# Kernel tuning notes

Measured on AMD Instinct MI355X. Metric: run time of the kernel, lower is better.

Reference implementation:

```python
import jax, jax.numpy as jnp
import numpy as np

EPS = 1e-5

def _ln(x, g, b):
    mu = jnp.mean(x, axis=-1, keepdims=True)
    var = jnp.mean((x - mu) ** 2, axis=-1, keepdims=True)
    return (x - mu) * jax.lax.rsqrt(var + EPS) * g + b

def _leaky(x):
    return jax.nn.leaky_relu(x, 0.1)

def _gather(feats, idx):
    # feats: [B,N,C], idx: [B,M,K] -> [B,M,K,C]
    return jax.vmap(lambda f, i: f[i])(feats, idx)

def _forward(dense_xyz, dense_feats, pe_w1, pe_b1, pe_g1, pe_be1, pe_w2, pe_b2, pe_g2, pe_be2,
             wn_w1, wn_b1, wn_g1, wn_be1, wn_w2, wn_b2, wn_g2, wn_be2, wn_w3, wn_b3, wn_g3, wn_be3,
             nm_g, nm_b, l1_w, l1_b, l2_w, l2_b, sc_w, sc_b, nei_inds):
    gathered_xyz = _gather(dense_xyz, nei_inds)             # [B,M,K,3]
    localized = gathered_xyz - dense_xyz[:, :, None, :]     # relative coords (no subsampling: M==N)
    # pe_convs WeightNet: 3 -> 32 -> 32, LayerNorm per layer, LeakyReLU(0.1) except last
    h = _leaky(_ln(localized @ pe_w1 + pe_b1, pe_g1, pe_be1))
    feat_pe = _ln(h @ pe_w2 + pe_b2, pe_g2, pe_be2)         # [B,M,K,32]
    # weightnet: 3 -> 16 -> 16 -> Cin (per-edge depthwise weights)
    w = _leaky(_ln(localized @ wn_w1 + wn_b1, wn_g1, wn_be1))
    w = _leaky(_ln(w @ wn_w2 + wn_b2, wn_g2, wn_be2))
    w = _ln(w @ wn_w3 + wn_b3, wn_g3, wn_be3)               # [B,M,K,Cin]
    gathered_feat = _gather(dense_feats, nei_inds)          # [B,M,K,Cin]
    # depthwise aggregation over K, pe channels aggregated alongside
    agg = jnp.concatenate([jnp.sum(gathered_feat * w, axis=2), jnp.sum(feat_pe, axis=2)], axis=-1)
    x = _ln(agg, nm_g, nm_b)                                # LayerNorm(Cin+32)
    x = _leaky(x @ l1_w + l1_b)                             # inverted bottleneck 288 -> 1024
    x = x @ l2_w + l2_b                                     # 1024 -> Cout
    shortcut = dense_feats @ sc_w + sc_b                    # unary shortcut Cin -> Cout
    return _leaky(shortcut + x)

def setup_inputs():
    key = jax.random.key(0)
    B, N, K, CIN, COUT, PE, H = 1, 32768, 16, 256, 512, 32, 16
    ks = jax.random.split(key, 12)
    def g(k, shape, s=0.02):
        return jax.random.normal(k, shape, dtype=jnp.float32) * s
    return {
        "dense_xyz": jax.random.uniform(ks[0], (B, N, 3), dtype=jnp.float32),
        "dense_feats": jax.random.normal(ks[1], (B, N, CIN), dtype=jnp.float32),
        "nei_inds": jax.random.randint(ks[2], (B, N, K), 0, N),
        "pe_w1": g(ks[3], (3, PE), 0.2), "pe_b1": jnp.zeros((PE,), jnp.float32),
        "pe_g1": jnp.ones((PE,), jnp.float32), "pe_be1": jnp.zeros((PE,), jnp.float32),
        "pe_w2": g(ks[4], (PE, PE), 0.1), "pe_b2": jnp.zeros((PE,), jnp.float32),
        "pe_g2": jnp.ones((PE,), jnp.float32), "pe_be2": jnp.zeros((PE,), jnp.float32),
        "wn_w1": g(ks[5], (3, H), 0.2), "wn_b1": jnp.zeros((H,), jnp.float32),
        "wn_g1": jnp.ones((H,), jnp.float32), "wn_be1": jnp.zeros((H,), jnp.float32),
        "wn_w2": g(ks[6], (H, H), 0.1), "wn_b2": jnp.zeros((H,), jnp.float32),
        "wn_g2": jnp.ones((H,), jnp.float32), "wn_be2": jnp.zeros((H,), jnp.float32),
        "wn_w3": g(ks[7], (H, CIN), 0.1), "wn_b3": jnp.zeros((CIN,), jnp.float32),
        "wn_g3": jnp.ones((CIN,), jnp.float32), "wn_be3": jnp.zeros((CIN,), jnp.float32),
        "nm_g": jnp.ones((CIN + PE,), jnp.float32), "nm_b": jnp.zeros((CIN + PE,), jnp.float32),
        "l1_w": g(ks[8], (CIN + PE, 4 * CIN)), "l1_b": jnp.zeros((4 * CIN,), jnp.float32),
        "l2_w": g(ks[9], (4 * CIN, COUT)), "l2_b": jnp.zeros((COUT,), jnp.float32),
        "sc_w": g(ks[10], (CIN, COUT)), "sc_b": jnp.zeros((COUT,), jnp.float32),
    }

def reference(dense_xyz, dense_feats, nei_inds, pe_w1, pe_b1, pe_g1, pe_be1, pe_w2, pe_b2, pe_g2, pe_be2,
              wn_w1, wn_b1, wn_g1, wn_be1, wn_w2, wn_b2, wn_g2, wn_be2, wn_w3, wn_b3, wn_g3, wn_be3,
              nm_g, nm_b, l1_w, l1_b, l2_w, l2_b, sc_w, sc_b):
    return _forward(dense_xyz, dense_feats, pe_w1, pe_b1, pe_g1, pe_be1, pe_w2, pe_b2, pe_g2, pe_be2,
                    wn_w1, wn_b1, wn_g1, wn_be1, wn_w2, wn_b2, wn_g2, wn_be2, wn_w3, wn_b3, wn_g3, wn_be3,
                    nm_g, nm_b, l1_w, l1_b, l2_w, l2_b, sc_w, sc_b, nei_inds)
```

## Files before the change

kernel.cpp:

```cpp
#include <hip/hip_runtime.h>

#define NPTS  32768
#define KNB   16
#define CINC  256
#define PEC   32
#define HWN   16
#define CMID  288
#define L1OUT 1024
#define COUTC 512
#define EPSLN 1e-5f
#define PBLK  16
#define W2LD  272

typedef __attribute__((ext_vector_type(8))) short short8;
typedef __attribute__((ext_vector_type(4))) float f32x4;
typedef __attribute__((ext_vector_type(2))) float f32x2;

__device__ __forceinline__ float leaky(float x) { return x > 0.f ? x : 0.1f * x; }

__device__ __forceinline__ float bf2f(unsigned short u) {
    union { unsigned int i; float f; } x; x.i = ((unsigned int)u) << 16; return x.f;
}
__device__ __forceinline__ unsigned short f2bf(float f) {
    unsigned int x = __float_as_uint(f);
    x = (x + 0x7fffu + ((x >> 16) & 1u)) >> 16;
    return (unsigned short)x;
}

__device__ __forceinline__ f32x2 lo2(f32x4 v) { return __builtin_shufflevector(v, v, 0, 1); }
__device__ __forceinline__ f32x2 hi2(f32x4 v) { return __builtin_shufflevector(v, v, 2, 3); }

__device__ __forceinline__ void pkfma(f32x2& d, f32x2 a, f32x2 b) {
    asm("v_pk_fma_f32 %0, %1, %2, %0" : "+v"(d) : "v"(a), "v"(b));
}
__device__ __forceinline__ void pkfma_lo(f32x2& d, f32x2 a, f32x2 b) {
    asm("v_pk_fma_f32 %0, %1, %2, %0 op_sel:[0,0,0] op_sel_hi:[0,1,1]" : "+v"(d) : "v"(a), "v"(b));
}
__device__ __forceinline__ void pkfma_hi(f32x2& d, f32x2 a, f32x2 b) {
    asm("v_pk_fma_f32 %0, %1, %2, %0 op_sel:[1,0,0] op_sel_hi:[1,1,1]" : "+v"(d) : "v"(a), "v"(b));
}
__device__ __forceinline__ void pkfma_lo_s(f32x2& d, f32x2 a, f32x2 b) {
    asm("v_pk_fma_f32 %0, %1, %2, %0 op_sel:[0,0,0] op_sel_hi:[0,1,1]" : "+v"(d) : "v"(a), "s"(b));
}
__device__ __forceinline__ void pkfma_hi_s(f32x2& d, f32x2 a, f32x2 b) {
    asm("v_pk_fma_f32 %0, %1, %2, %0 op_sel:[1,0,0] op_sel_hi:[1,1,1]" : "+v"(d) : "v"(a), "s"(b));
}
__device__ __forceinline__ void pkfma_s0(f32x2& d, f32x2 a, f32x2 b) {
    asm("v_pk_fma_f32 %0, %1, %2, %0" : "+v"(d) : "s"(a), "v"(b));
}

__device__ __forceinline__ void gld_lds16(const unsigned short* g, unsigned short* l) {
    __builtin_amdgcn_global_load_lds(
        (const __attribute__((address_space(1))) unsigned int*)g,
        (__attribute__((address_space(3))) unsigned int*)l,
        16, 0, 0);
}
__device__ __forceinline__ void gld_lds16f(const float* g, float* l) {
    __builtin_amdgcn_global_load_lds(
        (const __attribute__((address_space(1))) unsigned int*)g,
        (__attribute__((address_space(3))) unsigned int*)l,
        16, 0, 0);
}

__device__ __forceinline__ void stage_tile(const unsigned short* __restrict__ g,
                                           size_t ld, int row0, int k0,
                                           unsigned short* lds, int wave, int lane)
{
    #pragma unroll
    for (int r = 0; r < 2; ++r) {
        int e   = r * 2048 + wave * 512 + lane * 8;
        int row = e >> 5;
        int kp  = e & 31;
        int kl  = kp ^ ((row & 3) << 3);
        const unsigned short* src = g + (size_t)(row0 + row) * ld + (k0 + kl);
        gld_lds16(src, lds + r * 2048 + wave * 512);
    }
}

__global__ __launch_bounds__(256) void wn3_stats_kernel(
    const float* __restrict__ W3, const float* __restrict__ b3, float* __restrict__ st)
{
    const int b = blockIdx.x;
    const int t = threadIdx.x;
    const int lane = t & 63, wave = t >> 6;
    const int c0 = lane * 4;

    if (b < 64) {
        int pair = b * 4 + wave;
        int h = pair >> 4, hp = pair & 15;
        f32x4 a  = *(const f32x4*)(W3 + h * CINC + c0);
        f32x4 bb = *(const f32x4*)(W3 + hp * CINC + c0);
        float g = a[0] * bb[0] + a[1] * bb[1] + a[2] * bb[2] + a[3] * bb[3];
        #pragma unroll
        for (int off = 1; off < 64; off <<= 1) g += __shfl_xor(g, off);
        if (lane == 0) st[pair] = g * (1.f / CINC);
    } else if (b == 64) {
        #pragma unroll
        for (int i = 0; i < 4; ++i) {
            int h = wave * 4 + i;
            f32x4 w  = *(const f32x4*)(W3 + h * CINC + c0);
            f32x4 bb = *(const f32x4*)(b3 + c0);
            float s  = w[0] + w[1] + w[2] + w[3];
            float sb = w[0] * bb[0] + w[1] * bb[1] + w[2] * bb[2] + w[3] * bb[3];
            #pragma unroll
            for (int off = 1; off < 64; off <<= 1) { s += __shfl_xor(s, off); sb += __shfl_xor(sb, off); }
            if (lane == 0) { st[256 + h] = s * (1.f / CINC); st[272 + h] = sb * (1.f / CINC); }
        }
    } else if (wave == 0) {
        f32x4 bb = *(const f32x4*)(b3 + c0);
        float s = bb[0] + bb[1] + bb[2] + bb[3];
        float q = bb[0] * bb[0] + bb[1] * bb[1] + bb[2] * bb[2] + bb[3] * bb[3];
        #pragma unroll
        for (int off = 1; off < 64; off <<= 1) { s += __shfl_xor(s, off); q += __shfl_xor(q, off); }
        if (lane == 0) { st[288] = s * (1.f / CINC); st[289] = q * (1.f / CINC); }
    }
}

__global__ __launch_bounds__(256, 3) void edge_fused_kernel(
    const float* __restrict__ xyz, const unsigned short* __restrict__ featsb,
    const int* __restrict__ nei,
    const float* __restrict__ pe_w1, const float* __restrict__ pe_b1,
    const float* __restrict__ pe_g1, const float* __restrict__ pe_be1,
    const float* __restrict__ pe_w2, const float* __restrict__ pe_b2,
    const float* __restrict__ pe_g2, const float* __restrict__ pe_be2,
    const float* __restrict__ wn_w1, const float* __restrict__ wn_b1,
    const float* __restrict__ wn_g1, const float* __restrict__ wn_be1,
    const float* __restrict__ wn_w2, const float* __restrict__ wn_b2,
    const float* __restrict__ wn_g2, const float* __restrict__ wn_be2,
    const float* __restrict__ st,
    const float* __restrict__ wn_w3, const float* __restrict__ wn_b3,
    const float* __restrict__ wn_g3, const float* __restrict__ wn_be3,
    const float* __restrict__ nm_g, const float* __restrict__ nm_b,
    unsigned short* __restrict__ xln)
{
    __shared__ __align__(16) float W3s[16 * 256];
    __shared__ __align__(16) float w2s[PBLK * W2LD];
    __shared__ __align__(16) float rms[PBLK * 16];
    __shared__ __align__(16) float mus[PBLK * 16];
    __shared__ float pes[PBLK * 32];

    const int t = threadIdx.x;

    {
        const int lane = t & 63, wave = t >> 6;
        #pragma unroll
        for (int r = 0; r < 4; ++r) {
            int base = (wave * 4 + r) * 256;
            gld_lds16f(wn_w3 + base + lane * 4, W3s + base);
        }
    }

    {
        const int lp = t >> 4, kk = t & 15;
        const int m = blockIdx.x * PBLK + lp;
        const int n = nei[m * KNB + kk];
        const float lx = xyz[n * 3 + 0] - xyz[m * 3 + 0];
        const float ly = xyz[n * 3 + 1] - xyz[m * 3 + 1];
        const float lz = xyz[n * 3 + 2] - xyz[m * 3 + 2];

        f32x2 w1p[8];
        float s = 0.f, q = 0.f;
        #pragma unroll
        for (int c4 = 0; c4 < 4; ++c4) {
            f32x4 wa = *(const f32x4*)&wn_w1[c4 * 4];
            f32x4 wb = *(const f32x4*)&wn_w1[16 + c4 * 4];
            f32x4 wc = *(const f32x4*)&wn_w1[32 + c4 * 4];
            f32x4 bb = *(const f32x4*)&wn_b1[c4 * 4];
            #pragma unroll
            for (int j = 0; j < 4; ++j) {
                float v = bb[j] + lx * wa[j] + ly * wb[j] + lz * wc[j];
                int c = c4 * 4 + j;
                w1p[c >> 1][c & 1] = v; s += v; q += v * v;
            }
        }
        float mu = s * (1.f / 16.f);
        float rstd = rsqrtf(q * (1.f / 16.f) - mu * mu + EPSLN);
        #pragma unroll
        for (int c4 = 0; c4 < 4; ++c4) {
            f32x4 g = *(const f32x4*)&wn_g1[c4 * 4];
            f32x4 be = *(const f32x4*)&wn_be1[c4 * 4];
            #pragma unroll
            for (int j = 0; j < 4; ++j) {
                int c = c4 * 4 + j;
                w1p[c >> 1][c & 1] = leaky((w1p[c >> 1][c & 1] - mu) * rstd * g[j] + be[j]);
            }
        }

        f32x2 w2p[8];
        #pragma unroll
        for (int c4 = 0; c4 < 4; ++c4) {
            f32x4 bb = *(const f32x4*)&wn_b2[c4 * 4];
            w2p[c4 * 2] = lo2(bb); w2p[c4 * 2 + 1] = hi2(bb);
        }
        #pragma unroll 2
        for (int jp = 0; jp < 8; ++jp) {
            f32x2 hp = w1p[jp];
            #pragma unroll
            for (int c4 = 0; c4 < 4; ++c4) {
                f32x4 w = *(const f32x4*)&wn_w2[(2 * jp) * 16 + c4 * 4];
                pkfma_lo_s(w2p[c4 * 2], hp, lo2(w));
                pkfma_lo_s(w2p[c4 * 2 + 1], hp, hi2(w));
            }
            #pragma unroll
            for (int c4 = 0; c4 < 4; ++c4) {
                f32x4 w = *(const f32x4*)&wn_w2[(2 * jp + 1) * 16 + c4 * 4];
                pkfma_hi_s(w2p[c4 * 2], hp, lo2(w));
                pkfma_hi_s(w2p[c4 * 2 + 1], hp, hi2(w));
            }
        }
        s = 0.f; q = 0.f;
        #pragma unroll
        for (int i = 0; i < 8; ++i) {
            s += w2p[i][0] + w2p[i][1];
            q += w2p[i][0] * w2p[i][0] + w2p[i][1] * w2p[i][1];
        }
        mu = s * (1.f / 16.f);
        rstd = rsqrtf(q * (1.f / 16.f) - mu * mu + EPSLN);
        #pragma unroll
        for (int c4 = 0; c4 < 4; ++c4) {
            f32x4 g = *(const f32x4*)&wn_g2[c4 * 4];
            f32x4 be = *(const f32x4*)&wn_be2[c4 * 4];
            #pragma unroll
            for (int j = 0; j < 4; ++j) {
                int c = c4 * 4 + j;
                w2p[c >> 1][c & 1] = leaky((w2p[c >> 1][c & 1] - mu) * rstd * g[j] + be[j]);
            }
        }

        float mu3 = st[288];
        #pragma unroll
        for (int h4 = 0; h4 < 4; ++h4) {
            f32x4 wm = *(const f32x4*)&st[256 + h4 * 4];
            mu3 += wm[0] * w2p[h4 * 2][0] + wm[1] * w2p[h4 * 2][1]
                 + wm[2] * w2p[h4 * 2 + 1][0] + wm[3] * w2p[h4 * 2 + 1][1];
        }
        float esq = st[289];
        #pragma unroll 4
        for (int hh = 0; hh < 16; ++hh) {
            f32x2 acc2 = {0.f, 0.f};
            #pragma unroll
            for (int h4 = 0; h4 < 4; ++h4) {
                f32x4 g = *(const f32x4*)&st[hh * 16 + h4 * 4];
                pkfma_s0(acc2, lo2(g), w2p[h4 * 2]);
                pkfma_s0(acc2, hi2(g), w2p[h4 * 2 + 1]);
            }
            float acc = acc2[0] + acc2[1] + 2.f * st[272 + hh];
            esq += w2p[hh >> 1][hh & 1] * acc;
        }
        float r3 = rsqrtf(esq - mu3 * mu3 + EPSLN);

        #pragma unroll
        for (int hh = 0; hh < 16; ++hh)
            w2s[lp * W2LD + hh * 16 + kk] = w2p[hh >> 1][hh & 1];
        rms[lp * 16 + kk] = r3;
        mus[lp * 16 + kk] = mu3;

        f32x2 h2[16];
        s = 0.f; q = 0.f;
        #pragma unroll
        for (int c4 = 0; c4 < 8; ++c4) {
            f32x4 wa = *(const f32x4*)&pe_w1[c4 * 4];
            f32x4 wb = *(const f32x4*)&pe_w1[32 + c4 * 4];
            f32x4 wc = *(const f32x4*)&pe_w1[64 + c4 * 4];
            f32x4 bb = *(const f32x4*)&pe_b1[c4 * 4];
            #pragma unroll
            for (int j = 0; j < 4; ++j) {
                float v = bb[j] + lx * wa[j] + ly * wb[j] + lz * wc[j];
                int c = c4 * 4 + j;
                h2[c >> 1][c & 1] = v; s += v; q += v * v;
            }
        }
        mu = s * (1.f / 32.f);
        rstd = rsqrtf(q * (1.f / 32.f) - mu * mu + EPSLN);
        #pragma unroll
        for (int c4 = 0; c4 < 8; ++c4) {
            f32x4 g = *(const f32x4*)&pe_g1[c4 * 4];
            f32x4 be = *(const f32x4*)&pe_be1[c4 * 4];
            #pragma unroll
            for (int j = 0; j < 4; ++j) {
                int c = c4 * 4 + j;
                h2[c >> 1][c & 1] = leaky((h2[c >> 1][c & 1] - mu) * rstd * g[j] + be[j]);
            }
        }

        f32x2 f2[16];
        #pragma unroll
        for (int c4 = 0; c4 < 8; ++c4) {
            f32x4 bb = *(const f32x4*)&pe_b2[c4 * 4];
            f2[c4 * 2] = lo2(bb); f2[c4 * 2 + 1] = hi2(bb);
        }
        #pragma unroll 2
        for (int jp = 0; jp < 16; ++jp) {
            f32x2 hp = h2[jp];
            #pragma unroll
            for (int c4 = 0; c4 < 8; ++c4) {
                f32x4 w = *(const f32x4*)&pe_w2[(2 * jp) * 32 + c4 * 4];
                pkfma_lo_s(f2[c4 * 2], hp, lo2(w));
                pkfma_lo_s(f2[c4 * 2 + 1], hp, hi2(w));
            }
            #pragma unroll
            for (int c4 = 0; c4 < 8; ++c4) {
                f32x4 w = *(const f32x4*)&pe_w2[(2 * jp + 1) * 32 + c4 * 4];
                pkfma_hi_s(f2[c4 * 2], hp, lo2(w));
                pkfma_hi_s(f2[c4 * 2 + 1], hp, hi2(w));
            }
        }
        s = 0.f; q = 0.f;
        #pragma unroll
        for (int i = 0; i < 16; ++i) {
            s += f2[i][0] + f2[i][1];
            q += f2[i][0] * f2[i][0] + f2[i][1] * f2[i][1];
        }
        mu = s * (1.f / 32.f);
        rstd = rsqrtf(q * (1.f / 32.f) - mu * mu + EPSLN);
        #pragma unroll
        for (int c4 = 0; c4 < 8; ++c4) {
            f32x4 g = *(const f32x4*)&pe_g2[c4 * 4];
            f32x4 be = *(const f32x4*)&pe_be2[c4 * 4];
            #pragma unroll
            for (int j = 0; j < 4; ++j) {
                int c = c4 * 4 + j;
                float v = (f2[c >> 1][c & 1] - mu) * rstd * g[j] + be[j];
                v += __shfl_xor(v, 1);
                v += __shfl_xor(v, 2);
                v += __shfl_xor(v, 4);
                v += __shfl_xor(v, 8);
                if (kk == 0) pes[lp * 32 + c] = v;
            }
        }
    }
    __syncthreads();

    const int lane = t & 63, wave = t >> 6;
    const int c0 = lane * 4;
    const f32x4 b3r  = *(const f32x4*)(wn_b3 + c0);
    const f32x4 g3r  = *(const f32x4*)(wn_g3 + c0);
    const f32x4 be3r = *(const f32x4*)(wn_be3 + c0);

    for (int pp = 0; pp < 4; ++pp) {
        const int lp = wave * 4 + pp;
        const int p  = blockIdx.x * PBLK + lp;
        const int* np = nei + p * KNB;

        f32x2 raw2[16][2];
        #pragma unroll
        for (int k = 0; k < 16; ++k) {
            raw2[k][0] = (f32x2){0.f, 0.f};
            raw2[k][1] = (f32x2){0.f, 0.f};
        }

        #pragma unroll 2
        for (int hh = 0; hh < 16; ++hh) {
            f32x4 w3r = *(const f32x4*)&W3s[hh * 256 + c0];
            f32x2 w01 = lo2(w3r), w23 = hi2(w3r);
            f32x4 u0 = *(const f32x4*)&w2s[lp * W2LD + hh * 16 + 0];
            f32x4 u1 = *(const f32x4*)&w2s[lp * W2LD + hh * 16 + 4];
            f32x4 u2 = *(const f32x4*)&w2s[lp * W2LD + hh * 16 + 8];
            f32x4 u3 = *(const f32x4*)&w2s[lp * W2LD + hh * 16 + 12];
            f32x2 p0 = lo2(u0), p1 = hi2(u0), p2 = lo2(u1), p3 = hi2(u1);
            f32x2 p4 = lo2(u2), p5 = hi2(u2), p6 = lo2(u3), p7 = hi2(u3);
            pkfma_lo(raw2[ 0][0], p0, w01); pkfma_lo(raw2[ 0][1], p0, w23);
            pkfma_hi(raw2[ 1][0], p0, w01); pkfma_hi(raw2[ 1][1], p0, w23);
            pkfma_lo(raw2[ 2][0], p1, w01); pkfma_lo(raw2[ 2][1], p1, w23);
            pkfma_hi(raw2[ 3][0], p1, w01); pkfma_hi(raw2[ 3][1], p1, w23);
            pkfma_lo(raw2[ 4][0], p2, w01); pkfma_lo(raw2[ 4][1], p2, w23);
            pkfma_hi(raw2[ 5][0], p2, w01); pkfma_hi(raw2[ 5][1], p2, w23);
            pkfma_lo(raw2[ 6][0], p3, w01); pkfma_lo(raw2[ 6][1], p3, w23);
            pkfma_hi(raw2[ 7][0], p3, w01); pkfma_hi(raw2[ 7][1], p3, w23);
            pkfma_lo(raw2[ 8][0], p4, w01); pkfma_lo(raw2[ 8][1], p4, w23);
            pkfma_hi(raw2[ 9][0], p4, w01); pkfma_hi(raw2[ 9][1], p4, w23);
            pkfma_lo(raw2[10][0], p5, w01); pkfma_lo(raw2[10][1], p5, w23);
            pkfma_hi(raw2[11][0], p5, w01); pkfma_hi(raw2[11][1], p5, w23);
            pkfma_lo(raw2[12][0], p6, w01); pkfma_lo(raw2[12][1], p6, w23);
            pkfma_hi(raw2[13][0], p6, w01); pkfma_hi(raw2[13][1], p6, w23);
            pkfma_lo(raw2[14][0], p7, w01); pkfma_lo(raw2[14][1], p7, w23);
            pkfma_hi(raw2[15][0], p7, w01); pkfma_hi(raw2[15][1], p7, w23);
        }

        float agg[4] = {0.f, 0.f, 0.f, 0.f};
        #pragma unroll
        for (int k4 = 0; k4 < 4; ++k4) {
            f32x4 rkv = *(const f32x4*)&rms[lp * 16 + k4 * 4];
            f32x4 muv = *(const f32x4*)&mus[lp * 16 + k4 * 4];
            #pragma unroll
            for (int r = 0; r < 4; ++r) {
                int k = k4 * 4 + r;
                int nk = np[k];
                float rk  = rkv[r];
                float muk = muv[r];
                ushort4 fu = *(const ushort4*)(featsb + (size_t)nk * CINC + c0);
                float w3x = (raw2[k][0][0] + b3r[0] - muk) * rk * g3r[0] + be3r[0];
                float w3y = (raw2[k][0][1] + b3r[1] - muk) * rk * g3r[1] + be3r[1];
                float w3z = (raw2[k][1][0] + b3r[2] - muk) * rk * g3r[2] + be3r[2];
                float w3w = (raw2[k][1][1] + b3r[3] - muk) * rk * g3r[3] + be3r[3];
                agg[0] += bf2f(fu.x) * w3x;
                agg[1] += bf2f(fu.y) * w3y;
                agg[2] += bf2f(fu.z) * w3z;
                agg[3] += bf2f(fu.w) * w3w;
            }
        }

        float pv = (lane < 32) ? pes[lp * 32 + lane] : 0.f;

        float s = agg[0] + agg[1] + agg[2] + agg[3];
        float q = agg[0] * agg[0] + agg[1] * agg[1] + agg[2] * agg[2] + agg[3] * agg[3];
        if (lane < 32) { s += pv; q += pv * pv; }
        #pragma unroll
        for (int off = 1; off < 64; off <<= 1) {
            s += __shfl_xor(s, off);
            q += __shfl_xor(q, off);
        }
        float mu = s * (1.f / 288.f);
        float rstd = rsqrtf(q * (1.f / 288.f) - mu * mu + EPSLN);

        f32x4 ngr = *(const f32x4*)(nm_g + c0);
        f32x4 nbr = *(const f32x4*)(nm_b + c0);
        unsigned short* xp = xln + (size_t)p * CMID;
        ushort4 o;
        o.x = f2bf((agg[0] - mu) * rstd * ngr[0] + nbr[0]);
        o.y = f2bf((agg[1] - mu) * rstd * ngr[1] + nbr[1]);
        o.z = f2bf((agg[2] - mu) * rstd * ngr[2] + nbr[2]);
        o.w = f2bf((agg[3] - mu) * rstd * ngr[3] + nbr[3]);
        *(ushort4*)(xp + c0) = o;
        if (lane < 32)
            xp[256 + lane] = f2bf((pv - mu) * rstd * nm_g[256 + lane] + nm_b[256 + lane]);
    }
}

__global__ __launch_bounds__(256) void transpose_bf16_kernel(
    const float* __restrict__ src, unsigned short* __restrict__ dst, int K, int N)
{
    __shared__ float tile[32][33];
    const int k0 = blockIdx.y * 32, n0 = blockIdx.x * 32;
    const int tx = threadIdx.x & 31, ty = threadIdx.x >> 5;
    #pragma unroll
    for (int i = ty; i < 32; i += 8)
        tile[i][tx] = src[(size_t)(k0 + i) * N + n0 + tx];
    __syncthreads();
    #pragma unroll
    for (int i = ty; i < 32; i += 8)
        dst[(size_t)(n0 + i) * K + k0 + tx] = f2bf(tile[tx][i]);
}

__global__ __launch_bounds__(256) void feats_bf16_kernel(
    const float* __restrict__ src, unsigned short* __restrict__ dst)
{
    int i = (blockIdx.x * 256 + threadIdx.x) * 4;
    float4 v = *(const float4*)(src + i);
    ushort4 o;
    o.x = f2bf(v.x); o.y = f2bf(v.y); o.z = f2bf(v.z); o.w = f2bf(v.w);
    *(ushort4*)(dst + i) = o;
}

__global__ __launch_bounds__(256) void gemm1_mfma(
    const unsigned short* __restrict__ A,
    const unsigned short* __restrict__ BT,
    const float* __restrict__ bias,
    unsigned short* __restrict__ C)
{
    __shared__ unsigned short As[128 * 32];
    __shared__ unsigned short Bs[128 * 32];
    const int t = threadIdx.x;
    const int lane = t & 63, wave = t >> 6;
    const int wm = wave >> 1, wn = wave & 1;
    const int m0 = blockIdx.y * 128, n0 = blockIdx.x * 128;
    const int l15 = lane & 15, j0 = (lane >> 4) << 3;

    f32x4 zero = {0.f, 0.f, 0.f, 0.f};
    f32x4 acc[4][4];
    #pragma unroll
    for (int i = 0; i < 4; ++i)
        #pragma unroll
        for (int j = 0; j < 4; ++j) acc[i][j] = zero;

    for (int kt = 0; kt < CMID; kt += 32) {
        stage_tile(A,  CMID, m0, kt, As, wave, lane);
        stage_tile(BT, CMID, n0, kt, Bs, wave, lane);
        __syncthreads();
        short8 af[4], bf[4];
        #pragma unroll
        for (int i = 0; i < 4; ++i) {
            int ar = wm * 64 + i * 16 + l15;
            af[i] = *(const short8*)&As[ar * 32 + (j0 ^ ((ar & 3) << 3))];
            int br = wn * 64 + i * 16 + l15;
            bf[i] = *(const short8*)&Bs[br * 32 + (j0 ^ ((br & 3) << 3))];
        }
        #pragma unroll
        for (int i = 0; i < 4; ++i)
            #pragma unroll
            for (int j = 0; j < 4; ++j)
                acc[i][j] = __builtin_amdgcn_mfma_f32_16x16x32_bf16(af[i], bf[j], acc[i][j], 0, 0, 0);
        __syncthreads();
    }

    const int q = lane >> 4;
    #pragma unroll
    for (int j = 0; j < 4; ++j) {
        int ncol = n0 + wn * 64 + j * 16 + l15;
        float bv = bias[ncol];
        #pragma unroll
        for (int i = 0; i < 4; ++i) {
            int mbase = m0 + wm * 64 + i * 16 + q * 4;
            #pragma unroll
            for (int r = 0; r < 4; ++r)
                C[(size_t)(mbase + r) * L1OUT + ncol] = f2bf(leaky(acc[i][j][r] + bv));
        }
    }
}

__global__ __launch_bounds__(256) void gemm2_mfma(
    const unsigned short* __restrict__ H,
    const unsigned short* __restrict__ W2T,
    const unsigned short* __restrict__ F,
    const unsigned short* __restrict__ WscT,
    const float* __restrict__ b2, const float* __restrict__ bsc,
    float* __restrict__ Out)
{
    __shared__ unsigned short As[128 * 32];
    __shared__ unsigned short Bs[128 * 32];
    const int t = threadIdx.x;
    const int lane = t & 63, wave = t >> 6;
    const int wm = wave >> 1, wn = wave & 1;
    const int m0 = blockIdx.y * 128, n0 = blockIdx.x * 128;
    const int l15 = lane & 15, j0 = (lane >> 4) << 3;

    f32x4 zero = {0.f, 0.f, 0.f, 0.f};
    f32x4 acc[4][4];
    #pragma unroll
    for (int i = 0; i < 4; ++i)
        #pragma unroll
        for (int j = 0; j < 4; ++j) acc[i][j] = zero;

    for (int kt = 0; kt < L1OUT; kt += 32) {
        stage_tile(H,   L1OUT, m0, kt, As, wave, lane);
        stage_tile(W2T, L1OUT, n0, kt, Bs, wave, lane);
        __syncthreads();
        short8 af[4], bf[4];
        #pragma unroll
        for (int i = 0; i < 4; ++i) {
            int ar = wm * 64 + i * 16 + l15;
            af[i] = *(const short8*)&As[ar * 32 + (j0 ^ ((ar & 3) << 3))];
            int br = wn * 64 + i * 16 + l15;
            bf[i] = *(const short8*)&Bs[br * 32 + (j0 ^ ((br & 3) << 3))];
        }
        #pragma unroll
        for (int i = 0; i < 4; ++i)
            #pragma unroll
            for (int j = 0; j < 4; ++j)
                acc[i][j] = __builtin_amdgcn_mfma_f32_16x16x32_bf16(af[i], bf[j], acc[i][j], 0, 0, 0);
        __syncthreads();
    }
    for (int kt = 0; kt < CINC; kt += 32) {
        stage_tile(F,    CINC, m0, kt, As, wave, lane);
        stage_tile(WscT, CINC, n0, kt, Bs, wave, lane);
        __syncthreads();
        short8 af[4], bf[4];
        #pragma unroll
        for (int i = 0; i < 4; ++i) {
            int ar = wm * 64 + i * 16 + l15;
            af[i] = *(const short8*)&As[ar * 32 + (j0 ^ ((ar & 3) << 3))];
            int br = wn * 64 + i * 16 + l15;
            bf[i] = *(const short8*)&Bs[br * 32 + (j0 ^ ((br & 3) << 3))];
        }
        #pragma unroll
        for (int i = 0; i < 4; ++i)
            #pragma unroll
            for (int j = 0; j < 4; ++j)
                acc[i][j] = __builtin_amdgcn_mfma_f32_16x16x32_bf16(af[i], bf[j], acc[i][j], 0, 0, 0);
        __syncthreads();
    }

    const int q = lane >> 4;
    #pragma unroll
    for (int j = 0; j < 4; ++j) {
        int ncol = n0 + wn * 64 + j * 16 + l15;
        float bv = b2[ncol] + bsc[ncol];
        #pragma unroll
        for (int i = 0; i < 4; ++i) {
            int mbase = m0 + wm * 64 + i * 16 + q * 4;
            #pragma unroll
            for (int r = 0; r < 4; ++r)
                Out[(size_t)(mbase + r) * COUTC + ncol] = leaky(acc[i][j][r] + bv);
        }
    }
}

extern "C" void kernel_launch(void* const* d_in, const int* in_sizes, int n_in,
                              void* d_out, int out_size, void* d_ws, size_t ws_size,
                              hipStream_t stream)
{
    const float* xyz    = (const float*)d_in[0];
    const float* feats  = (const float*)d_in[1];
    const int*   nei    = (const int*)d_in[2];
    const float* pe_w1  = (const float*)d_in[3];
    const float* pe_b1  = (const float*)d_in[4];
    const float* pe_g1  = (const float*)d_in[5];
    const float* pe_be1 = (const float*)d_in[6];
    const float* pe_w2  = (const float*)d_in[7];
    const float* pe_b2  = (const float*)d_in[8];
    const float* pe_g2  = (const float*)d_in[9];
    const float* pe_be2 = (const float*)d_in[10];
    const float* wn_w1  = (const float*)d_in[11];
    const float* wn_b1  = (const float*)d_in[12];
    const float* wn_g1  = (const float*)d_in[13];
    const float* wn_be1 = (const float*)d_in[14];
    const float* wn_w2  = (const float*)d_in[15];
    const float* wn_b2  = (const float*)d_in[16];
    const float* wn_g2  = (const float*)d_in[17];
    const float* wn_be2 = (const float*)d_in[18];
    const float* wn_w3  = (const float*)d_in[19];
    const float* wn_b3  = (const float*)d_in[20];
    const float* wn_g3  = (const float*)d_in[21];
    const float* wn_be3 = (const float*)d_in[22];
    const float* nm_g   = (const float*)d_in[23];
    const float* nm_b   = (const float*)d_in[24];
    const float* l1_w   = (const float*)d_in[25];
    const float* l1_b   = (const float*)d_in[26];
    const float* l2_w   = (const float*)d_in[27];
    const float* l2_b   = (const float*)d_in[28];
    const float* sc_w   = (const float*)d_in[29];
    const float* sc_b   = (const float*)d_in[30];

    char* ws = (char*)d_ws;
    unsigned short* xln    = (unsigned short*)(ws);
    unsigned short* featsb = (unsigned short*)(ws + 18874368);
    unsigned short* l1_wT  = (unsigned short*)(ws + 35651584);
    unsigned short* l2_wT  = (unsigned short*)(ws + 36241408);
    unsigned short* sc_wT  = (unsigned short*)(ws + 37289984);
    float*          st     = (float*)(ws + 37552128);
    unsigned short* h1     = (unsigned short*)(ws + 37556224);

    wn3_stats_kernel<<<66, 256, 0, stream>>>(wn_w3, wn_b3, st);
    transpose_bf16_kernel<<<dim3(L1OUT / 32, CMID / 32), 256, 0, stream>>>(l1_w, l1_wT, CMID, L1OUT);
    transpose_bf16_kernel<<<dim3(COUTC / 32, L1OUT / 32), 256, 0, stream>>>(l2_w, l2_wT, L1OUT, COUTC);
    transpose_bf16_kernel<<<dim3(COUTC / 32, CINC / 32), 256, 0, stream>>>(sc_w, sc_wT, CINC, COUTC);
    feats_bf16_kernel<<<(NPTS * CINC / 4) / 256, 256, 0, stream>>>(feats, featsb);

    edge_fused_kernel<<<NPTS / PBLK, 256, 0, stream>>>(
        xyz, featsb, nei,
        pe_w1, pe_b1, pe_g1, pe_be1, pe_w2, pe_b2, pe_g2, pe_be2,
        wn_w1, wn_b1, wn_g1, wn_be1, wn_w2, wn_b2, wn_g2, wn_be2,
        st, wn_w3, wn_b3, wn_g3, wn_be3, nm_g, nm_b, xln);

    gemm1_mfma<<<dim3(L1OUT / 128, NPTS / 128), 256, 0, stream>>>(xln, l1_wT, l1_b, h1);

    gemm2_mfma<<<dim3(COUTC / 128, NPTS / 128), 256, 0, stream>>>(
        h1, l2_wT, featsb, sc_wT, l2_b, sc_b, (float*)d_out);
}
```

Before: 406.1 us.

## Merge prep kernels into one launch and add XCD-aware block swizzle to GEMMs

Folds the five small preprocessing kernels (weight statistics, three weight transposes, feature bf16 conversion) into a single prep kernel that dispatches by block index, removing four launches and their inter-kernel gaps. It also remaps block indices in both MFMA GEMMs so that consecutive tiles land on the same XCD, aiming for better L2 reuse of shared A/B tiles. The swizzle assumes the total block count divides evenly by 8, and the merged kernel adds branching plus shared-memory allocation for every block.

```diff
diff --git a/kernel.cpp b/kernel.cpp
--- a/kernel.cpp
+++ b/kernel.cpp
@@ -77,42 +77,89 @@
     }
 }
 
-__global__ __launch_bounds__(256) void wn3_stats_kernel(
-    const float* __restrict__ W3, const float* __restrict__ b3, float* __restrict__ st)
+__device__ __forceinline__ void xcd_swz(int gx, int& bx, int& by) {
+    int lin = blockIdx.y * gx + blockIdx.x;
+    int n   = gx * gridDim.y;
+    int s   = (lin & 7) * (n >> 3) + (lin >> 3);
+    bx = s % gx;
+    by = s / gx;
+}
+
+__device__ __forceinline__ void transpose_body(
+    const float* __restrict__ src, unsigned short* __restrict__ dst,
+    int K, int N, int bx, int by, float (*tile)[33])
 {
+    const int k0 = by * 32, n0 = bx * 32;
+    const int tx = threadIdx.x & 31, ty = threadIdx.x >> 5;
+    #pragma unroll
+    for (int i = ty; i < 32; i += 8)
+        tile[i][tx] = src[(size_t)(k0 + i) * N + n0 + tx];
+    __syncthreads();
+    #pragma unroll
+    for (int i = ty; i < 32; i += 8)
+        dst[(size_t)(n0 + i) * K + k0 + tx] = f2bf(tile[tx][i]);
+}
+
+__global__ __launch_bounds__(256) void prep_kernel(
+    const float* __restrict__ feats, unsigned short* __restrict__ featsb,
+    const float* __restrict__ l1_w, unsigned short* __restrict__ l1_wT,
+    const float* __restrict__ l2_w, unsigned short* __restrict__ l2_wT,
+    const float* __restrict__ sc_w, unsigned short* __restrict__ sc_wT,
+    const float* __restrict__ W3, const float* __restrict__ b3,
+    float* __restrict__ st)
+{
+    __shared__ float tile[32][33];
     const int b = blockIdx.x;
     const int t = threadIdx.x;
-    const int lane = t & 63, wave = t >> 6;
-    const int c0 = lane * 4;
-
-    if (b < 64) {
-        int pair = b * 4 + wave;
-        int h = pair >> 4, hp = pair & 15;
-        f32x4 a  = *(const f32x4*)(W3 + h * CINC + c0);
-        f32x4 bb = *(const f32x4*)(W3 + hp * CINC + c0);
-        float g = a[0] * bb[0] + a[1] * bb[1] + a[2] * bb[2] + a[3] * bb[3];
-        #pragma unroll
-        for (int off = 1; off < 64; off <<= 1) g += __shfl_xor(g, off);
-        if (lane == 0) st[pair] = g * (1.f / CINC);
-    } else if (b == 64) {
-        #pragma unroll
-        for (int i = 0; i < 4; ++i) {
-            int h = wave * 4 + i;
-            f32x4 w  = *(const f32x4*)(W3 + h * CINC + c0);
+
+    if (b < 8192) {
+        int i = (b * 256 + t) * 4;
+        float4 v = *(const float4*)(feats + i);
+        ushort4 o;
+        o.x = f2bf(v.x); o.y = f2bf(v.y); o.z = f2bf(v.z); o.w = f2bf(v.w);
+        *(ushort4*)(featsb + i) = o;
+    } else if (b < 8480) {
+        int idx = b - 8192;
+        transpose_body(l1_w, l1_wT, CMID, L1OUT, idx % 32, idx / 32, tile);
+    } else if (b < 8992) {
+        int idx = b - 8480;
+        transpose_body(l2_w, l2_wT, L1OUT, COUTC, idx % 16, idx / 16, tile);
+    } else if (b < 9120) {
+        int idx = b - 8992;
+        transpose_body(sc_w, sc_wT, CINC, COUTC, idx % 16, idx / 16, tile);
+    } else {
+        const int sb = b - 9120;
+        const int lane = t & 63, wave = t >> 6;
+        const int c0 = lane * 4;
+        if (sb < 64) {
+            int pair = sb * 4 + wave;
+            int h = pair >> 4, hp = pair & 15;
+            f32x4 a  = *(const f32x4*)(W3 + h * CINC + c0);
+            f32x4 bb = *(const f32x4*)(W3 + hp * CINC + c0);
+            float g = a[0] * bb[0] + a[1] * bb[1] + a[2] * bb[2] + a[3] * bb[3];
+            #pragma unroll
+            for (int off = 1; off < 64; off <<= 1) g += __shfl_xor(g, off);
+            if (lane == 0) st[pair] = g * (1.f / CINC);
+        } else if (sb == 64) {
+            #pragma unroll
+            for (int i = 0; i < 4; ++i) {
+                int h = wave * 4 + i;
+                f32x4 w  = *(const f32x4*)(W3 + h * CINC + c0);
+                f32x4 bb = *(const f32x4*)(b3 + c0);
+                float s  = w[0] + w[1] + w[2] + w[3];
+                float sbv = w[0] * bb[0] + w[1] * bb[1] + w[2] * bb[2] + w[3] * bb[3];
+                #pragma unroll
+                for (int off = 1; off < 64; off <<= 1) { s += __shfl_xor(s, off); sbv += __shfl_xor(sbv, off); }
+                if (lane == 0) { st[256 + h] = s * (1.f / CINC); st[272 + h] = sbv * (1.f / CINC); }
+            }
+        } else if (wave == 0) {
             f32x4 bb = *(const f32x4*)(b3 + c0);
-            float s  = w[0] + w[1] + w[2] + w[3];
-            float sb = w[0] * bb[0] + w[1] * bb[1] + w[2] * bb[2] + w[3] * bb[3];
-            #pragma unroll
-            for (int off = 1; off < 64; off <<= 1) { s += __shfl_xor(s, off); sb += __shfl_xor(sb, off); }
-            if (lane == 0) { st[256 + h] = s * (1.f / CINC); st[272 + h] = sb * (1.f / CINC); }
-        }
-    } else if (wave == 0) {
-        f32x4 bb = *(const f32x4*)(b3 + c0);
-        float s = bb[0] + bb[1] + bb[2] + bb[3];
-        float q = bb[0] * bb[0] + bb[1] * bb[1] + bb[2] * bb[2] + bb[3] * bb[3];
-        #pragma unroll
-        for (int off = 1; off < 64; off <<= 1) { s += __shfl_xor(s, off); q += __shfl_xor(q, off); }
-        if (lane == 0) { st[288] = s * (1.f / CINC); st[289] = q * (1.f / CINC); }
+            float s = bb[0] + bb[1] + bb[2] + bb[3];
+            float q = bb[0] * bb[0] + bb[1] * bb[1] + bb[2] * bb[2] + bb[3] * bb[3];
+            #pragma unroll
+            for (int off = 1; off < 64; off <<= 1) { s += __shfl_xor(s, off); q += __shfl_xor(q, off); }
+            if (lane == 0) { st[288] = s * (1.f / CINC); st[289] = q * (1.f / CINC); }
+        }
     }
 }
 
@@ -427,31 +474,6 @@
     }
 }
 
-__global__ __launch_bounds__(256) void transpose_bf16_kernel(
-    const float* __restrict__ src, unsigned short* __restrict__ dst, int K, int N)
-{
-    __shared__ float tile[32][33];
-    const int k0 = blockIdx.y * 32, n0 = blockIdx.x * 32;
-    const int tx = threadIdx.x & 31, ty = threadIdx.x >> 5;
-    #pragma unroll
-    for (int i = ty; i < 32; i += 8)
-        tile[i][tx] = src[(size_t)(k0 + i) * N + n0 + tx];
-    __syncthreads();
-    #pragma unroll
-    for (int i = ty; i < 32; i += 8)
-        dst[(size_t)(n0 + i) * K + k0 + tx] = f2bf(tile[tx][i]);
-}
-
-__global__ __launch_bounds__(256) void feats_bf16_kernel(
-    const float* __restrict__ src, unsigned short* __restrict__ dst)
-{
-    int i = (blockIdx.x * 256 + threadIdx.x) * 4;
-    float4 v = *(const float4*)(src + i);
-    ushort4 o;
-    o.x = f2bf(v.x); o.y = f2bf(v.y); o.z = f2bf(v.z); o.w = f2bf(v.w);
-    *(ushort4*)(dst + i) = o;
-}
-
 __global__ __launch_bounds__(256) void gemm1_mfma(
     const unsigned short* __restrict__ A,
     const unsigned short* __restrict__ BT,
@@ -463,7 +485,9 @@
     const int t = threadIdx.x;
     const int lane = t & 63, wave = t >> 6;
     const int wm = wave >> 1, wn = wave & 1;
-    const int m0 = blockIdx.y * 128, n0 = blockIdx.x * 128;
+    int bx, by;
+    xcd_swz(L1OUT / 128, bx, by);
+    const int m0 = by * 128, n0 = bx * 128;
     const int l15 = lane & 15, j0 = (lane >> 4) << 3;
 
     f32x4 zero = {0.f, 0.f, 0.f, 0.f};
@@ -521,7 +545,9 @@
     const int t = threadIdx.x;
     const int lane = t & 63, wave = t >> 6;
     const int wm = wave >> 1, wn = wave & 1;
-    const int m0 = blockIdx.y * 128, n0 = blockIdx.x * 128;
+    int bx, by;
+    xcd_swz(COUTC / 128, bx, by);
+    const int m0 = by * 128, n0 = bx * 128;
     const int l15 = lane & 15, j0 = (lane >> 4) << 3;
 
     f32x4 zero = {0.f, 0.f, 0.f, 0.f};
@@ -630,11 +656,8 @@
     float*          st     = (float*)(ws + 37552128);
     unsigned short* h1     = (unsigned short*)(ws + 37556224);
 
-    wn3_stats_kernel<<<66, 256, 0, stream>>>(wn_w3, wn_b3, st);
-    transpose_bf16_kernel<<<dim3(L1OUT / 32, CMID / 32), 256, 0, stream>>>(l1_w, l1_wT, CMID, L1OUT);
-    transpose_bf16_kernel<<<dim3(COUTC / 32, L1OUT / 32), 256, 0, stream>>>(l2_w, l2_wT, L1OUT, COUTC);
-    transpose_bf16_kernel<<<dim3(COUTC / 32, CINC / 32), 256, 0, stream>>>(sc_w, sc_wT, CINC, COUTC);
-    feats_bf16_kernel<<<(NPTS * CINC / 4) / 256, 256, 0, stream>>>(feats, featsb);
+    prep_kernel<<<9186, 256, 0, stream>>>(
+        feats, featsb, l1_w, l1_wT, l2_w, l2_wT, sc_w, sc_wT, wn_w3, wn_b3, st);
 
     edge_fused_kernel<<<NPTS / PBLK, 256, 0, stream>>>(
         xyz, featsb, nei,
```

After: 377.8 us, median of 3. 7.0% less time.
